# Performance work log

Measured on AMD Instinct MI355X. Metric: run time of the kernel, lower is better.

The kernel has to match this reference:

```python
import jax, jax.numpy as jnp
import numpy as np

N_INPUTS = 64
N_OUTPUTS = 64
N_OPS = 8  # ('none','linear','power_two','power_three','exp','ln','reciprocal','sin')
BATCH = 65536
TEMP = 1.0


def setup_inputs() -> dict:
    key = jax.random.key(0)
    k1, k2, k3 = jax.random.split(key, 3)
    # shift inputs into (0.5, 1.5) so ln / reciprocal are well-behaved
    x = jax.random.uniform(k1, (BATCH, N_INPUTS), dtype=jnp.float32) + 0.5
    alphas = 0.001 * jax.random.normal(k2, (N_INPUTS, N_OUTPUTS, N_OPS), dtype=jnp.float32)
    coeffs = jax.random.normal(k3, (N_INPUTS, N_OUTPUTS, N_OPS), dtype=jnp.float32)
    return {"x": x, "alphas": alphas, "coeffs": coeffs}


def _primitives(x):
    # x: [B, I] -> [B, I, N_OPS], one channel per primitive op
    return jnp.stack(
        [
            jnp.zeros_like(x),   # none
            x,                   # linear
            x * x,               # power_two
            x * x * x,           # power_three
            jnp.exp(x),          # exp
            jnp.log(x),          # ln
            1.0 / x,             # reciprocal
            jnp.sin(x),          # sin
        ],
        axis=-1,
    )


def reference(x, alphas, coeffs):
    # softmax gating over primitives (non-discrete, non-gumbel branch)
    gates = jax.nn.softmax(alphas / TEMP, axis=-1)        # [I, J, K]
    prims = _primitives(x)                                # [B, I, K]
    # operation_outputs[b,i,j] = sum_k gates[i,j,k] * coeffs[i,j,k] * prims[b,i,k]
    # layer_output[b,j] = sum_i operation_outputs[b,i,j]
    w = gates * coeffs                                    # [I, J, K]
    out = jnp.einsum("bik,ijk->bj", prims, w)            # [B, J]
    return out
```

## Files before the change

### kernel.cpp

```cpp
#include <hip/hip_runtime.h>
#include <hip/hip_bf16.h>
#include <stdint.h>


typedef __bf16 bf16x8 __attribute__((ext_vector_type(8)));
typedef float f32x4 __attribute__((ext_vector_type(4)));

typedef __attribute__((address_space(1))) void gvoid;
typedef __attribute__((address_space(3))) void lvoid;

__device__ __forceinline__ void async16(const void* g, void* l) {
    __builtin_amdgcn_global_load_lds((gvoid*)g, (lvoid*)l, 16, 0, 0);
}

__global__ void build_w(const float* __restrict__ alphas,
                        const float* __restrict__ coeffs,
                        __bf16* __restrict__ w2) {
    int gid = blockIdx.x * blockDim.x + threadIdx.x;
    int i = gid >> 6;
    int n = gid & 63;
    const float* a = alphas + gid * 8;
    const float* c = coeffs + gid * 8;

    float av[8], mx = -1e30f;
#pragma unroll
    for (int k = 0; k < 8; ++k) { av[k] = a[k]; mx = fmaxf(mx, av[k]); }
    float e[8], s = 0.f;
#pragma unroll
    for (int k = 0; k < 8; ++k) { e[k] = __expf(av[k] - mx); s += e[k]; }
    float inv = 1.0f / s;

    bf16x8 w;
#pragma unroll
    for (int k = 0; k < 8; ++k) w[k] = (__bf16)(e[k] * inv * c[k]);

    int q = i >> 4, cc = i & 15, t = n >> 4, nl = n & 15;
    int pos = ((cc * 4 + t) * 64 + q * 16 + nl) * 8;
    *(bf16x8*)(w2 + pos) = w;
}

__global__ __launch_bounds__(512, 4) void darts_main(const float* __restrict__ x,
                                                     const __bf16* __restrict__ w2,
                                                     float* __restrict__ out) {
    __shared__ __bf16 wlds[32768];

    const int tid  = threadIdx.x;
    const int lane = tid & 63;
    const int wv   = tid >> 6;
    const int m    = lane & 15;
    const int q    = lane >> 4;

    const int row = blockIdx.x * 128 + wv * 16 + m;
    const float* xp = x + row * 64 + q * 16;
    f32x4 xr0 = *(const f32x4*)(xp + 0);
    f32x4 xr1 = *(const f32x4*)(xp + 4);
    f32x4 xr2 = *(const f32x4*)(xp + 8);
    f32x4 xr3 = *(const f32x4*)(xp + 12);

#pragma unroll
    for (int it = 0; it < 8; ++it) {
        async16((const char*)w2 + (it * 512 + tid) * 16,
                (char*)wlds + it * 8192 + wv * 1024);
    }
    __syncthreads();

    float xa[16];
#pragma unroll
    for (int c = 0; c < 4; ++c) { xa[c] = xr0[c]; xa[4+c] = xr1[c]; xa[8+c] = xr2[c]; xa[12+c] = xr3[c]; }

    f32x4 acc0 = {0.f, 0.f, 0.f, 0.f};
    f32x4 acc1 = {0.f, 0.f, 0.f, 0.f};
    f32x4 acc2 = {0.f, 0.f, 0.f, 0.f};
    f32x4 acc3 = {0.f, 0.f, 0.f, 0.f};

#pragma unroll
    for (int c = 0; c < 16; ++c) {
        float xv = xa[c];
        float x2 = xv * xv;
        bf16x8 a;
        a[0] = (__bf16)0.0f;
        a[1] = (__bf16)xv;
        a[2] = (__bf16)x2;
        a[3] = (__bf16)(x2 * xv);
        a[4] = (__bf16)__expf(xv);
        a[5] = (__bf16)__logf(xv);
        a[6] = (__bf16)__builtin_amdgcn_rcpf(xv);
        a[7] = (__bf16)__sinf(xv);

        const __bf16* bb = wlds + c * 2048 + lane * 8;
        bf16x8 b0 = *(const bf16x8*)(bb);
        bf16x8 b1 = *(const bf16x8*)(bb + 512);
        bf16x8 b2 = *(const bf16x8*)(bb + 1024);
        bf16x8 b3 = *(const bf16x8*)(bb + 1536);
        acc0 = __builtin_amdgcn_mfma_f32_16x16x32_bf16(a, b0, acc0, 0, 0, 0);
        acc1 = __builtin_amdgcn_mfma_f32_16x16x32_bf16(a, b1, acc1, 0, 0, 0);
        acc2 = __builtin_amdgcn_mfma_f32_16x16x32_bf16(a, b2, acc2, 0, 0, 0);
        acc3 = __builtin_amdgcn_mfma_f32_16x16x32_bf16(a, b3, acc3, 0, 0, 0);
    }

    float* orow = out + (blockIdx.x * 128 + wv * 16 + q * 4) * 64 + m;
#pragma unroll
    for (int r = 0; r < 4; ++r) {
        orow[r * 64 + 0]  = acc0[r];
        orow[r * 64 + 16] = acc1[r];
        orow[r * 64 + 32] = acc2[r];
        orow[r * 64 + 48] = acc3[r];
    }
}

extern "C" void kernel_launch(void* const* d_in, const int* in_sizes, int n_in,
                              void* d_out, int out_size, void* d_ws, size_t ws_size,
                              hipStream_t stream) {
    const float* x      = (const float*)d_in[0];
    const float* alphas = (const float*)d_in[1];
    const float* coeffs = (const float*)d_in[2];
    float* out = (float*)d_out;
    __bf16* w2 = (__bf16*)d_ws;

    build_w<<<16, 256, 0, stream>>>(alphas, coeffs, w2);
    darts_main<<<512, 512, 0, stream>>>(x, w2, out);
}
```

Baseline: 78.73 us.

## Fuse softmax weight construction into main kernel, dropping separate prep launch

Removes the separate build_w kernel and has every block of the main kernel compute the softmax-gated, coefficient-scaled bf16 weights directly into LDS from alphas and coeffs. This saves a kernel launch and the workspace round trip. In exchange, each of the 512 blocks redoes the full 64x64x8 softmax and reads both fp32 tensors, which is twice the bytes of the bf16 workspace, instead of issuing async global-to-LDS copies.

```diff
diff --git a/kernel.cpp b/kernel.cpp
--- a/kernel.cpp
+++ b/kernel.cpp
@@ -6,42 +6,10 @@
 typedef __bf16 bf16x8 __attribute__((ext_vector_type(8)));
 typedef float f32x4 __attribute__((ext_vector_type(4)));
 
-typedef __attribute__((address_space(1))) void gvoid;
-typedef __attribute__((address_space(3))) void lvoid;
-
-__device__ __forceinline__ void async16(const void* g, void* l) {
-    __builtin_amdgcn_global_load_lds((gvoid*)g, (lvoid*)l, 16, 0, 0);
-}
-
-__global__ void build_w(const float* __restrict__ alphas,
-                        const float* __restrict__ coeffs,
-                        __bf16* __restrict__ w2) {
-    int gid = blockIdx.x * blockDim.x + threadIdx.x;
-    int i = gid >> 6;
-    int n = gid & 63;
-    const float* a = alphas + gid * 8;
-    const float* c = coeffs + gid * 8;
-
-    float av[8], mx = -1e30f;
-#pragma unroll
-    for (int k = 0; k < 8; ++k) { av[k] = a[k]; mx = fmaxf(mx, av[k]); }
-    float e[8], s = 0.f;
-#pragma unroll
-    for (int k = 0; k < 8; ++k) { e[k] = __expf(av[k] - mx); s += e[k]; }
-    float inv = 1.0f / s;
-
-    bf16x8 w;
-#pragma unroll
-    for (int k = 0; k < 8; ++k) w[k] = (__bf16)(e[k] * inv * c[k]);
-
-    int q = i >> 4, cc = i & 15, t = n >> 4, nl = n & 15;
-    int pos = ((cc * 4 + t) * 64 + q * 16 + nl) * 8;
-    *(bf16x8*)(w2 + pos) = w;
-}
-
-__global__ __launch_bounds__(512, 4) void darts_main(const float* __restrict__ x,
-                                                     const __bf16* __restrict__ w2,
-                                                     float* __restrict__ out) {
+__global__ __launch_bounds__(512, 4) void darts_fused(const float* __restrict__ x,
+                                                      const float* __restrict__ alphas,
+                                                      const float* __restrict__ coeffs,
+                                                      float* __restrict__ out) {
     __shared__ __bf16 wlds[32768];
 
     const int tid  = threadIdx.x;
@@ -58,9 +26,27 @@
     f32x4 xr3 = *(const f32x4*)(xp + 12);
 
 #pragma unroll
-    for (int it = 0; it < 8; ++it) {
-        async16((const char*)w2 + (it * 512 + tid) * 16,
-                (char*)wlds + it * 8192 + wv * 1024);
+    for (int u = 0; u < 8; ++u) {
+        const int g = u * 512 + tid;
+        const int i = g >> 6;
+        const int n = g & 63;
+        const float* a  = alphas + g * 8;
+        const float* cf = coeffs + g * 8;
+
+        float av[8], mx = -1e30f;
+#pragma unroll
+        for (int k = 0; k < 8; ++k) { av[k] = a[k]; mx = fmaxf(mx, av[k]); }
+        float e[8], s = 0.f;
+#pragma unroll
+        for (int k = 0; k < 8; ++k) { e[k] = __expf(av[k] - mx); s += e[k]; }
+        const float inv = 1.0f / s;
+
+        bf16x8 w;
+#pragma unroll
+        for (int k = 0; k < 8; ++k) w[k] = (__bf16)(e[k] * inv * cf[k]);
+
+        const int qq = i >> 4, cc = i & 15, t = n >> 4, nl = n & 63 & 15;
+        *(bf16x8*)(wlds + ((cc * 4 + t) * 64 + qq * 16 + nl) * 8) = w;
     }
     __syncthreads();
 
@@ -75,8 +61,8 @@
 
 #pragma unroll
     for (int c = 0; c < 16; ++c) {
-        float xv = xa[c];
-        float x2 = xv * xv;
+        const float xv = xa[c];
+        const float x2 = xv * xv;
         bf16x8 a;
         a[0] = (__bf16)0.0f;
         a[1] = (__bf16)xv;
@@ -115,8 +101,7 @@
     const float* alphas = (const float*)d_in[1];
     const float* coeffs = (const float*)d_in[2];
     float* out = (float*)d_out;
-    __bf16* w2 = (__bf16*)d_ws;
+    (void)d_ws; (void)ws_size;
 
-    build_w<<<16, 256, 0, stream>>>(alphas, coeffs, w2);
-    darts_main<<<512, 512, 0, stream>>>(x, w2, out);
+    darts_fused<<<512, 512, 0, stream>>>(x, alphas, coeffs, out);
 }
```

After: 81.19 us. +3.1%, slower.

## Drop LDS staging; split output columns across waves, weights loaded into registers

Applied to the files above, without the earlier changes.

Removes the shared-memory staging of the weight matrix and the block barrier. Each wave now owns one 16-column slice of the output for a 16-row tile and loads its weight fragments straight from global memory (L2-resident) into registers. The grid becomes 4096 blocks of 256 threads. In exchange, every wave recomputes the transcendental primitives for the same rows, four times more in total, and issues more global weight loads.

```diff
diff --git a/kernel.cpp b/kernel.cpp
--- a/kernel.cpp
+++ b/kernel.cpp
@@ -5,13 +5,6 @@
 
 typedef __bf16 bf16x8 __attribute__((ext_vector_type(8)));
 typedef float f32x4 __attribute__((ext_vector_type(4)));
-
-typedef __attribute__((address_space(1))) void gvoid;
-typedef __attribute__((address_space(3))) void lvoid;
-
-__device__ __forceinline__ void async16(const void* g, void* l) {
-    __builtin_amdgcn_global_load_lds((gvoid*)g, (lvoid*)l, 16, 0, 0);
-}
 
 __global__ void build_w(const float* __restrict__ alphas,
                         const float* __restrict__ coeffs,
@@ -39,44 +32,38 @@
     *(bf16x8*)(w2 + pos) = w;
 }
 
-__global__ __launch_bounds__(512, 4) void darts_main(const float* __restrict__ x,
+__global__ __launch_bounds__(256, 4) void darts_main(const float* __restrict__ x,
                                                      const __bf16* __restrict__ w2,
                                                      float* __restrict__ out) {
-    __shared__ __bf16 wlds[32768];
-
     const int tid  = threadIdx.x;
     const int lane = tid & 63;
     const int wv   = tid >> 6;
     const int m    = lane & 15;
     const int q    = lane >> 4;
 
-    const int row = blockIdx.x * 128 + wv * 16 + m;
+    const int row = blockIdx.x * 16 + m;
     const float* xp = x + row * 64 + q * 16;
     f32x4 xr0 = *(const f32x4*)(xp + 0);
     f32x4 xr1 = *(const f32x4*)(xp + 4);
     f32x4 xr2 = *(const f32x4*)(xp + 8);
     f32x4 xr3 = *(const f32x4*)(xp + 12);
 
+    bf16x8 bf[16];
 #pragma unroll
-    for (int it = 0; it < 8; ++it) {
-        async16((const char*)w2 + (it * 512 + tid) * 16,
-                (char*)wlds + it * 8192 + wv * 1024);
+    for (int c = 0; c < 16; ++c) {
+        bf[c] = *(const bf16x8*)(w2 + ((c * 4 + wv) * 64 + lane) * 8);
     }
-    __syncthreads();
 
     float xa[16];
 #pragma unroll
     for (int c = 0; c < 4; ++c) { xa[c] = xr0[c]; xa[4+c] = xr1[c]; xa[8+c] = xr2[c]; xa[12+c] = xr3[c]; }
 
-    f32x4 acc0 = {0.f, 0.f, 0.f, 0.f};
-    f32x4 acc1 = {0.f, 0.f, 0.f, 0.f};
-    f32x4 acc2 = {0.f, 0.f, 0.f, 0.f};
-    f32x4 acc3 = {0.f, 0.f, 0.f, 0.f};
+    f32x4 acc = {0.f, 0.f, 0.f, 0.f};
 
 #pragma unroll
     for (int c = 0; c < 16; ++c) {
-        float xv = xa[c];
-        float x2 = xv * xv;
+        const float xv = xa[c];
+        const float x2 = xv * xv;
         bf16x8 a;
         a[0] = (__bf16)0.0f;
         a[1] = (__bf16)xv;
@@ -86,25 +73,13 @@
         a[5] = (__bf16)__logf(xv);
         a[6] = (__bf16)__builtin_amdgcn_rcpf(xv);
         a[7] = (__bf16)__sinf(xv);
-
-        const __bf16* bb = wlds + c * 2048 + lane * 8;
-        bf16x8 b0 = *(const bf16x8*)(bb);
-        bf16x8 b1 = *(const bf16x8*)(bb + 512);
-        bf16x8 b2 = *(const bf16x8*)(bb + 1024);
-        bf16x8 b3 = *(const bf16x8*)(bb + 1536);
-        acc0 = __builtin_amdgcn_mfma_f32_16x16x32_bf16(a, b0, acc0, 0, 0, 0);
-        acc1 = __builtin_amdgcn_mfma_f32_16x16x32_bf16(a, b1, acc1, 0, 0, 0);
-        acc2 = __builtin_amdgcn_mfma_f32_16x16x32_bf16(a, b2, acc2, 0, 0, 0);
-        acc3 = __builtin_amdgcn_mfma_f32_16x16x32_bf16(a, b3, acc3, 0, 0, 0);
+        acc = __builtin_amdgcn_mfma_f32_16x16x32_bf16(a, bf[c], acc, 0, 0, 0);
     }
 
-    float* orow = out + (blockIdx.x * 128 + wv * 16 + q * 4) * 64 + m;
+    float* orow = out + (blockIdx.x * 16 + q * 4) * 64 + wv * 16 + m;
 #pragma unroll
     for (int r = 0; r < 4; ++r) {
-        orow[r * 64 + 0]  = acc0[r];
-        orow[r * 64 + 16] = acc1[r];
-        orow[r * 64 + 32] = acc2[r];
-        orow[r * 64 + 48] = acc3[r];
+        orow[r * 64] = acc[r];
     }
 }
 
@@ -118,5 +93,5 @@
     __bf16* w2 = (__bf16*)d_ws;
 
     build_w<<<16, 256, 0, stream>>>(alphas, coeffs, w2);
-    darts_main<<<512, 512, 0, stream>>>(x, w2, out);
+    darts_main<<<4096, 256, 0, stream>>>(x, w2, out);
 }
```

Measured after the change: 86.74 us. 10.2% more time.
